# Kernel optimization log

Measured on AMD Instinct MI355X. Metric: run time of the kernel, lower is better.

The kernel has to match this reference:

```python
import jax, jax.numpy as jnp
import numpy as np

T = 128        # number of time points
D = 64         # flattened state dim (bs * z_dim, bs = 1)
H = 256        # hidden width of f-network
HK = 128       # hidden width of kernel network
MAX_IT = 3     # fixed-point iterations (args.max_iterations)


def setup_inputs() -> dict:
    key = jax.random.key(0)
    ks = jax.random.split(key, 6)
    g = lambda k, sh, sc: (jax.random.normal(k, sh, jnp.float32) * sc)
    z0 = jax.random.normal(ks[0], (1, D), jnp.float32)
    t = jnp.linspace(0.0, 1.0, T, dtype=jnp.float32)
    # f: D -> H -> D MLP (the 'func' integrand network)
    W1 = g(ks[1], (D, H), 1.0 / np.sqrt(D)); b1 = jnp.zeros((H,), jnp.float32)
    W2 = g(ks[2], (H, D), 1.0 / np.sqrt(H)); b2 = jnp.zeros((D,), jnp.float32)
    # kernel: (x, s) -> D*D matrix entries (the neural kernel K)
    Wk1 = g(ks[3], (2, HK), 1.0 / np.sqrt(2.0)); bk1 = jnp.zeros((HK,), jnp.float32)
    Wk2 = g(ks[4], (HK, D * D), 1.0 / np.sqrt(HK)); bk2 = jnp.zeros((D * D,), jnp.float32)
    return dict(z0=z0, t=t, W1=W1, b1=b1, W2=W2, b2=b2,
                Wk1=Wk1, bk1=bk1, Wk2=Wk2, bk2=bk2)


def _trapezoid_weights(t):
    """w[i, j]: trapezoid quadrature weight of node j for integral over [t0, t_i]."""
    dt = t[1] - t[0]  # uniform grid
    idx = jnp.arange(T)
    mask = (idx[None, :] <= idx[:, None]).astype(t.dtype)
    w = dt * mask
    w = w.at[(idx, idx)].multiply(0.5)   # halve right endpoint of each row
    w = w.at[:, 0].multiply(0.5)         # halve left endpoint
    w = w.at[0].set(0.0)                 # zero-length integral at t0
    return w


def _solve(z0, t, W1, b1, W2, b2, Wk1, bk1, Wk2, bk2):
    y0 = z0.reshape(-1)                                   # [D], solver flattens batch
    w = _trapezoid_weights(t)                             # [T, T]
    # Neural kernel K(x_i, s_j) -> [D, D], precomputed once on the grid.
    pairs = jnp.stack([jnp.broadcast_to(t[:, None], (T, T)),
                       jnp.broadcast_to(t[None, :], (T, T))], axis=-1)  # [T, T, 2]
    hK = jnp.tanh(pairs @ Wk1 + bk1)                      # [T, T, HK]
    K = (hK @ Wk2 + bk2).reshape(T, T, D, D)              # [T, T, D, D]

    def f(y):  # integrand network, applied over all time points
        return jnp.tanh(y @ W1 + b1) @ W2 + b2            # [T, D]

    def step(y, _):
        # G_i = \int_0^{x_i} K(x_i, s) f(y(s)) ds  (trapezoid on grid)
        G = jnp.einsum('ij,ijde,je->id', w, K, f(y))      # [T, D]
        # y'(x) = G(x)  =>  y_i = y0 + \int_0^{x_i} G(s) ds
        y_new = y0[None, :] + w @ G                       # [T, D]
        return y_new, None

    y_init = jnp.tile(y0[None, :], (T, 1))                # fixed-point initial guess
    y, _ = jax.lax.scan(step, y_init, None, length=MAX_IT)
    return y


def reference(z0, t, W1, b1, W2, b2, Wk1, bk1, Wk2, bk2):
    y = _solve(z0, t, W1, b1, W2, b2, Wk1, bk1, Wk2, bk2)  # [T, D]
    return y[-1].reshape(1, D)  # z[-1]: final state, shape [bs, dim]
```

## Files before the change

### kernel.cpp

```cpp
#include <hip/hip_runtime.h>
#include <hip/hip_bf16.h>

#define TT 128
#define DD 64
#define HH 256
#define HK 128
#define JH (TT*HK)
#define HD (HK*DD)
#define NCHUNK 64

__global__ void __launch_bounds__(256)
k_F0M0(const float* __restrict__ z0,
       const float* __restrict__ W1, const float* __restrict__ b1,
       const float* __restrict__ W2, const float* __restrict__ b2,
       const float* __restrict__ bk2, const float* __restrict__ Wk2,
       float* __restrict__ M0, float* __restrict__ bF0) {
    int bx = blockIdx.x, tid = threadIdx.x;
    int part = tid >> 6, d = tid & 63;
    __shared__ float red[4][64];
    __shared__ float ys[DD];
    __shared__ float hs[HH];
    __shared__ __attribute__((aligned(16))) float fs[DD];
    if (tid < DD) ys[tid] = z0[tid];
    __syncthreads();
    float acc = b1[tid];
    #pragma unroll 8
    for (int e = 0; e < DD; ++e) acc += ys[e] * W1[e * HH + tid];
    hs[tid] = tanhf(acc);
    __syncthreads();
    {
        float s = 0.f;
        #pragma unroll 8
        for (int h = part * 64; h < part * 64 + 64; ++h) s += hs[h] * W2[h * DD + d];
        red[part][d] = s;
    }
    __syncthreads();
    if (part == 0)
        fs[d] = b2[d] + red[0][d] + red[1][d] + red[2][d] + red[3][d];
    __syncthreads();
    if (bx == 0) {
        float s = 0.f;
        #pragma unroll
        for (int e = part * 16; e < part * 16 + 16; ++e) s += bk2[d * DD + e] * fs[e];
        red[part][d] = s;
        __syncthreads();
        if (part == 0)
            bF0[d] = red[0][d] + red[1][d] + red[2][d] + red[3][d];
    }
    int hd = bx * 256 + tid;
    const float* Wrow = Wk2 + (size_t)(hd >> 6) * (DD * DD) + (size_t)(hd & 63) * DD;
    float a = 0.f;
    #pragma unroll
    for (int e = 0; e < DD; e += 8) {
        float4 wa = *(const float4*)(Wrow + e);
        float4 wb = *(const float4*)(Wrow + e + 4);
        float4 fa = *(const float4*)&fs[e];
        float4 fb = *(const float4*)&fs[e + 4];
        a += fa.x*wa.x + fa.y*wa.y + fa.z*wa.z + fa.w*wa.w
           + fb.x*wb.x + fb.y*wb.y + fb.z*wb.z + fb.w*wb.w;
    }
    M0[hd] = a;
}

__global__ void __launch_bounds__(256)
k_G0(const float* __restrict__ t, const float* __restrict__ Wk1,
     const float* __restrict__ bk1, const float* __restrict__ M0,
     const float* __restrict__ bF0, float* __restrict__ G) {
    int i = blockIdx.x, tid = threadIdx.x;
    int part = tid >> 6, d = tid & 63;
    __shared__ float Bpart[2][HK];
    __shared__ float Bs[HK];
    __shared__ float red[4][64];
    float dt = t[1] - t[0];
    int h = tid & 127, half = tid >> 7;
    float b = 0.f;
    if (i > 0) {
        float wk0 = Wk1[h], wk1v = Wk1[HK + h], bk = bk1[h];
        float ti = t[i];
        for (int j = half; j <= i; j += 2) {
            float w = dt * ((j == 0 || j == i) ? 0.5f : 1.0f);
            b += w * tanhf(ti * wk0 + t[j] * wk1v + bk);
        }
    }
    Bpart[half][h] = b;
    __syncthreads();
    if (tid < HK) Bs[tid] = Bpart[0][tid] + Bpart[1][tid];
    __syncthreads();
    float a = 0.f;
    #pragma unroll 8
    for (int h2 = part * 32; h2 < part * 32 + 32; ++h2)
        a += Bs[h2] * M0[h2 * DD + d];
    red[part][d] = a;
    __syncthreads();
    if (part == 0) {
        float g = red[0][d] + red[1][d] + red[2][d] + red[3][d];
        if (i > 0) g += dt * (float)i * bF0[d];
        G[i * DD + d] = g;
    }
}

__global__ void __launch_bounds__(256)
k_F(const float* __restrict__ G, const float* __restrict__ z0,
    const float* __restrict__ t,
    const float* __restrict__ W1, const float* __restrict__ b1,
    const float* __restrict__ W2, const float* __restrict__ b2,
    const float* __restrict__ bk2,
    float* __restrict__ F, float* __restrict__ bF) {
    int j = blockIdx.x, tid = threadIdx.x;
    int part = tid >> 6, d = tid & 63;
    __shared__ float red[4][64];
    __shared__ float ys[DD];
    __shared__ float hs[HH];
    __shared__ float fs[DD];
    float dt = t[1] - t[0];
    {
        float s = 0.f;
        if (j > 0) {
            for (int jp = part; jp <= j; jp += 4) {
                float w = (jp == 0 || jp == j) ? 0.5f : 1.0f;
                s += w * G[jp * DD + d];
            }
        }
        red[part][d] = s;
        __syncthreads();
        if (part == 0)
            ys[d] = z0[d] + dt * (red[0][d] + red[1][d] + red[2][d] + red[3][d]);
    }
    __syncthreads();
    float acc = b1[tid];
    #pragma unroll 8
    for (int e = 0; e < DD; ++e) acc += ys[e] * W1[e * HH + tid];
    hs[tid] = tanhf(acc);
    __syncthreads();
    {
        float s = 0.f;
        #pragma unroll 8
        for (int h = part * 64; h < part * 64 + 64; ++h) s += hs[h] * W2[h * DD + d];
        red[part][d] = s;
    }
    __syncthreads();
    if (part == 0) {
        float a = b2[d] + red[0][d] + red[1][d] + red[2][d] + red[3][d];
        fs[d] = a;
        F[j * DD + d] = a;
    }
    __syncthreads();
    {
        float s = 0.f;
        #pragma unroll
        for (int e = part * 16; e < part * 16 + 16; ++e) s += bk2[d * DD + e] * fs[e];
        red[part][d] = s;
    }
    __syncthreads();
    if (part == 0)
        bF[j * DD + d] = red[0][d] + red[1][d] + red[2][d] + red[3][d];
}

__global__ void __launch_bounds__(256)
k_M(const float* __restrict__ F, const float* __restrict__ Wk2,
    float* __restrict__ M) {
    int tid = threadIdx.x;
    int hd = blockIdx.x * 256 + tid;
    int j0 = blockIdx.y * 8;
    __shared__ __attribute__((aligned(16))) float Fs[8][64];
    for (int k = tid; k < 8 * DD; k += 256) Fs[k >> 6][k & 63] = F[j0 * DD + k];
    __syncthreads();
    float acc[8] = {0.f,0.f,0.f,0.f,0.f,0.f,0.f,0.f};
    const float* Wrow = Wk2 + (size_t)(hd >> 6) * (DD * DD) + (size_t)(hd & 63) * DD;
    for (int e = 0; e < DD; e += 8) {
        float4 wa = *(const float4*)(Wrow + e);
        float4 wb = *(const float4*)(Wrow + e + 4);
        #pragma unroll
        for (int r = 0; r < 8; ++r) {
            float4 f0 = *(const float4*)&Fs[r][e];
            float4 f1 = *(const float4*)&Fs[r][e + 4];
            acc[r] += f0.x*wa.x + f0.y*wa.y + f0.z*wa.z + f0.w*wa.w
                    + f1.x*wb.x + f1.y*wb.y + f1.z*wb.z + f1.w*wb.w;
        }
    }
    #pragma unroll
    for (int r = 0; r < 8; ++r) M[(size_t)(j0 + r) * HD + hd] = acc[r];
}

__global__ void __launch_bounds__(256)
k_G1(const float* __restrict__ t, const float* __restrict__ Wk1,
     const float* __restrict__ bk1, const float* __restrict__ M,
     float* __restrict__ P, const float* __restrict__ z0,
     float* __restrict__ out, int final_it) {
    int itile = blockIdx.x, c = blockIdx.y;
    if (c > 4 * itile + 3) return;
    __shared__ __attribute__((aligned(16))) float As[8 * 256];
    __shared__ float red[4][8][64];
    int tid = threadIdx.x, sub = tid >> 6, d = tid & 63;

    {
        float dt = t[1] - t[0];
        int h = tid & 127;
        int j = 2 * c + (tid >> 7);
        float wk0 = Wk1[h], wk1v = Wk1[HK + h], bk = bk1[h];
        float tj = t[j];
        #pragma unroll
        for (int k = 0; k < 8; ++k) {
            int i = itile * 8 + k;
            float w = (i == 0 || j > i) ? 0.f : dt * ((j == 0 || j == i) ? 0.5f : 1.0f);
            As[k * 256 + tid] = w * tanhf(t[i] * wk0 + tj * wk1v + bk);
        }
    }
    if (final_it && itile == 0 && c == 0 && tid < DD) out[tid] = z0[tid];
    __syncthreads();

    float acc[8] = {0.f,0.f,0.f,0.f,0.f,0.f,0.f,0.f};
    const float* Mp = M + ((size_t)c * 256) * DD + d;
    int jl0 = sub * 64;
    for (int jl = jl0; jl < jl0 + 64; jl += 8) {
        float m0 = Mp[(size_t)(jl + 0) * DD];
        float m1 = Mp[(size_t)(jl + 1) * DD];
        float m2 = Mp[(size_t)(jl + 2) * DD];
        float m3 = Mp[(size_t)(jl + 3) * DD];
        float m4 = Mp[(size_t)(jl + 4) * DD];
        float m5 = Mp[(size_t)(jl + 5) * DD];
        float m6 = Mp[(size_t)(jl + 6) * DD];
        float m7 = Mp[(size_t)(jl + 7) * DD];
        #pragma unroll
        for (int r = 0; r < 8; ++r) {
            float4 a0 = *(const float4*)&As[r * 256 + jl];
            float4 a1 = *(const float4*)&As[r * 256 + jl + 4];
            acc[r] += a0.x*m0 + a0.y*m1 + a0.z*m2 + a0.w*m3
                    + a1.x*m4 + a1.y*m5 + a1.z*m6 + a1.w*m7;
        }
    }
    #pragma unroll
    for (int r = 0; r < 8; ++r) red[sub][r][d] = acc[r];
    __syncthreads();
    if (sub == 0) {
        #pragma unroll
        for (int r = 0; r < 8; ++r) {
            float v = red[0][r][d] + red[1][r][d] + red[2][r][d] + red[3][r][d];
            P[(size_t)c * (TT * DD) + (itile * 8 + r) * DD + d] = v;
        }
    }
}

__global__ void __launch_bounds__(256)
k_Gfin(const float* __restrict__ P, const float* __restrict__ bF,
       const float* __restrict__ t, float* __restrict__ G,
       float* __restrict__ out, int final_it) {
    int j = blockIdx.x, tid = threadIdx.x;
    int part = tid >> 6, d = tid & 63;
    __shared__ float red[4][64];
    float dt = t[1] - t[0];
    float a = 0.f;
    int cmax = j >> 1;
    for (int c = part; c <= cmax; c += 4) a += P[(size_t)c * (TT * DD) + j * DD + d];
    if (j > 0) {
        float s = 0.f;
        for (int jp = part; jp <= j; jp += 4) {
            float w = (jp == 0 || jp == j) ? 0.5f : 1.0f;
            s += w * bF[jp * DD + d];
        }
        a += dt * s;
    }
    red[part][d] = a;
    __syncthreads();
    if (part == 0) {
        float v = red[0][d] + red[1][d] + red[2][d] + red[3][d];
        G[j * DD + d] = v;
        if (final_it) {
            float wj = (j == 0 || j == TT - 1) ? 0.5f : 1.0f;
            atomicAdd(&out[d], dt * wj * v);
        }
    }
}

extern "C" void kernel_launch(void* const* d_in, const int* in_sizes, int n_in,
                              void* d_out, int out_size, void* d_ws, size_t ws_size,
                              hipStream_t stream) {
    const float* z0  = (const float*)d_in[0];
    const float* t   = (const float*)d_in[1];
    const float* W1  = (const float*)d_in[2];
    const float* b1  = (const float*)d_in[3];
    const float* W2  = (const float*)d_in[4];
    const float* b2  = (const float*)d_in[5];
    const float* Wk1 = (const float*)d_in[6];
    const float* bk1 = (const float*)d_in[7];
    const float* Wk2 = (const float*)d_in[8];
    const float* bk2 = (const float*)d_in[9];
    float* out = (float*)d_out;

    float* ws  = (float*)d_ws;
    float* M   = ws;
    float* F   = M   + (size_t)TT*HK*DD;
    float* bF  = F   + TT*DD;
    float* G   = bF  + TT*DD;
    float* P   = G   + TT*DD;
    float* M0  = P   + (size_t)NCHUNK*TT*DD;
    float* bF0 = M0  + HD;

    k_F0M0<<<32, 256, 0, stream>>>(z0, W1, b1, W2, b2, bk2, Wk2, M0, bF0);
    k_G0<<<TT, 256, 0, stream>>>(t, Wk1, bk1, M0, bF0, G);
    for (int it = 1; it < 3; ++it) {
        int fin = (it == 2) ? 1 : 0;
        k_F<<<TT, 256, 0, stream>>>(G, z0, t, W1, b1, W2, b2, bk2, F, bF);
        k_M<<<dim3(32, 16), 256, 0, stream>>>(F, Wk2, M);
        k_G1<<<dim3(16, NCHUNK), 256, 0, stream>>>(t, Wk1, bk1, M, P, z0, out, fin);
        k_Gfin<<<TT, 256, 0, stream>>>(P, bF, t, G, out, fin);
    }
}
```

Measured before the change: 185.7 us.

## Fuse all stages into one cooperative persistent kernel with grid syncs

Replaces the sequence of ten kernel launches with a single cooperative kernel of 256 blocks that moves between stages using grid-wide barriers. The tanh kernel-feature tensor A (T×T×HK) is now computed once up front and kept in workspace, so the G0 and G1 stages read it instead of recomputing tanh in every iteration. The aim is to remove launch overhead and the repeated transcendental work. In exchange it adds grid.sync costs, a large extra workspace buffer that must be read back from memory, and less parallelism in some stages because of the fixed block count. The old multi-kernel path stays as a fallback if the cooperative launch fails.

```diff
diff --git a/kernel.cpp b/kernel.cpp
--- a/kernel.cpp
+++ b/kernel.cpp
@@ -1,13 +1,254 @@
 #include <hip/hip_runtime.h>
-#include <hip/hip_bf16.h>
+#include <hip/hip_cooperative_groups.h>
+
+namespace cg = cooperative_groups;
 
 #define TT 128
 #define DD 64
 #define HH 256
-#define HK 128
-#define JH (TT*HK)
-#define HD (HK*DD)
+#define HKD 128
+#define HD (HKD*DD)
 #define NCHUNK 64
+#define NBLK 256
+
+union __attribute__((aligned(16))) SharedU {
+    struct { float red[4][64]; float ys[DD]; float hs[HH]; float fs[DD]; } f;
+    struct { float Bpart[2][HKD]; float Bs[HKD]; float red[4][64]; } g0;
+    struct { float Fs[8][DD]; } m;
+    struct { float As[8 * 256]; float red[4][8][64]; } g1;
+};
+
+__device__ __forceinline__ void mlp_f(SharedU& sm, int tid,
+                                      const float* __restrict__ W1, const float* __restrict__ b1,
+                                      const float* __restrict__ W2, const float* __restrict__ b2) {
+    int part = tid >> 6, d = tid & 63;
+    float acc = b1[tid];
+    #pragma unroll 8
+    for (int e = 0; e < DD; ++e) acc += sm.f.ys[e] * W1[e * HH + tid];
+    sm.f.hs[tid] = tanhf(acc);
+    __syncthreads();
+    float s = 0.f;
+    #pragma unroll 8
+    for (int h = part * 64; h < part * 64 + 64; ++h) s += sm.f.hs[h] * W2[h * DD + d];
+    sm.f.red[part][d] = s;
+    __syncthreads();
+    if (part == 0)
+        sm.f.fs[d] = b2[d] + sm.f.red[0][d] + sm.f.red[1][d] + sm.f.red[2][d] + sm.f.red[3][d];
+    __syncthreads();
+}
+
+__device__ __forceinline__ float bk2dot(SharedU& sm, int tid, const float* __restrict__ bk2) {
+    int part = tid >> 6, d = tid & 63;
+    float s = 0.f;
+    #pragma unroll
+    for (int e = part * 16; e < part * 16 + 16; ++e) s += bk2[d * DD + e] * sm.f.fs[e];
+    sm.f.red[part][d] = s;
+    __syncthreads();
+    return sm.f.red[0][d] + sm.f.red[1][d] + sm.f.red[2][d] + sm.f.red[3][d];
+}
+
+extern "C" __global__ void __launch_bounds__(256, 2)
+mega(const float* __restrict__ z0, const float* __restrict__ t,
+     const float* __restrict__ W1, const float* __restrict__ b1,
+     const float* __restrict__ W2, const float* __restrict__ b2,
+     const float* __restrict__ Wk1, const float* __restrict__ bk1,
+     const float* __restrict__ Wk2, const float* __restrict__ bk2,
+     float* __restrict__ A, float* __restrict__ M,
+     float* __restrict__ F, float* __restrict__ bF,
+     float* __restrict__ G, float* __restrict__ P,
+     float* __restrict__ M0, float* __restrict__ bF0,
+     float* __restrict__ out)
+{
+    cg::grid_group grid = cg::this_grid();
+    const int b = blockIdx.x, tid = threadIdx.x;
+    const int part = tid >> 6, d = tid & 63;
+    __shared__ SharedU sm;
+    const float dt = t[1] - t[0];
+
+    if (b < 32) {
+        if (tid < DD) sm.f.ys[tid] = z0[tid];
+        __syncthreads();
+        mlp_f(sm, tid, W1, b1, W2, b2);
+        if (b == 0) {
+            float v = bk2dot(sm, tid, bk2);
+            if (part == 0) bF0[d] = v;
+        }
+        int hd = b * 256 + tid;
+        const float* Wrow = Wk2 + (size_t)(hd >> 6) * (DD * DD) + (size_t)(hd & 63) * DD;
+        float a = 0.f;
+        #pragma unroll
+        for (int e = 0; e < DD; e += 8) {
+            float4 wa = *(const float4*)(Wrow + e);
+            float4 wb = *(const float4*)(Wrow + e + 4);
+            float4 fa = *(const float4*)&sm.f.fs[e];
+            float4 fb = *(const float4*)&sm.f.fs[e + 4];
+            a += fa.x*wa.x + fa.y*wa.y + fa.z*wa.z + fa.w*wa.w
+               + fb.x*wb.x + fb.y*wb.y + fb.z*wb.z + fb.w*wb.w;
+        }
+        M0[hd] = a;
+    }
+    {
+        const int h = tid & 127;
+        const float wk0 = Wk1[h], wk1v = Wk1[HKD + h], bk = bk1[h];
+        const int base = b * (TT * TT * HKD / NBLK);
+        #pragma unroll 4
+        for (int k = 0; k < TT * TT * HKD / NBLK / 256; ++k) {
+            int n = base + k * 256 + tid;
+            int i = n >> 14, j = (n >> 7) & 127;
+            float w = (i == 0 || j > i) ? 0.f : dt * ((j == 0 || j == i) ? 0.5f : 1.f);
+            float v = 0.f;
+            if (w != 0.f)
+                v = w * tanhf(t[i] * wk0 + t[j] * wk1v + bk);
+            A[n] = v;
+        }
+    }
+    grid.sync();
+
+    if (b < TT) {
+        const int i = b;
+        const int h = tid & 127, half = tid >> 7;
+        float bsum = 0.f;
+        const float* Ai = A + (size_t)i * (TT * HKD);
+        for (int j = half; j <= i; j += 2) bsum += Ai[j * HKD + h];
+        sm.g0.Bpart[half][h] = bsum;
+        __syncthreads();
+        if (tid < HKD) sm.g0.Bs[tid] = sm.g0.Bpart[0][tid] + sm.g0.Bpart[1][tid];
+        __syncthreads();
+        float a = 0.f;
+        #pragma unroll 8
+        for (int h2 = part * 32; h2 < part * 32 + 32; ++h2) a += sm.g0.Bs[h2] * M0[h2 * DD + d];
+        sm.g0.red[part][d] = a;
+        __syncthreads();
+        if (part == 0) {
+            float g = sm.g0.red[0][d] + sm.g0.red[1][d] + sm.g0.red[2][d] + sm.g0.red[3][d];
+            if (i > 0) g += dt * (float)i * bF0[d];
+            G[i * DD + d] = g;
+        }
+    }
+    grid.sync();
+
+    for (int it = 1; it < 3; ++it) {
+        const int fin = (it == 2);
+
+        if (b < TT) {
+            const int j = b;
+            float s = 0.f;
+            if (j > 0) {
+                for (int jp = part; jp <= j; jp += 4) {
+                    float w = (jp == 0 || jp == j) ? 0.5f : 1.0f;
+                    s += w * G[jp * DD + d];
+                }
+            }
+            sm.f.red[part][d] = s;
+            __syncthreads();
+            if (part == 0)
+                sm.f.ys[d] = z0[d] + dt * (sm.f.red[0][d] + sm.f.red[1][d] + sm.f.red[2][d] + sm.f.red[3][d]);
+            __syncthreads();
+            mlp_f(sm, tid, W1, b1, W2, b2);
+            if (part == 0) F[j * DD + d] = sm.f.fs[d];
+            float v = bk2dot(sm, tid, bk2);
+            if (part == 0) bF[j * DD + d] = v;
+        }
+        grid.sync();
+
+        for (int u = b; u < 512; u += NBLK) {
+            const int hd = (u & 31) * 256 + tid;
+            const int j0 = (u >> 5) * 8;
+            __syncthreads();
+            for (int k2 = tid; k2 < 8 * DD; k2 += 256) sm.m.Fs[k2 >> 6][k2 & 63] = F[j0 * DD + k2];
+            __syncthreads();
+            float acc[8] = {0.f,0.f,0.f,0.f,0.f,0.f,0.f,0.f};
+            const float* Wrow = Wk2 + (size_t)(hd >> 6) * (DD * DD) + (size_t)(hd & 63) * DD;
+            for (int e = 0; e < DD; e += 8) {
+                float4 wa = *(const float4*)(Wrow + e);
+                float4 wb = *(const float4*)(Wrow + e + 4);
+                #pragma unroll
+                for (int r = 0; r < 8; ++r) {
+                    float4 f0 = *(const float4*)&sm.m.Fs[r][e];
+                    float4 f1 = *(const float4*)&sm.m.Fs[r][e + 4];
+                    acc[r] += f0.x*wa.x + f0.y*wa.y + f0.z*wa.z + f0.w*wa.w
+                            + f1.x*wb.x + f1.y*wb.y + f1.z*wb.z + f1.w*wb.w;
+                }
+            }
+            #pragma unroll
+            for (int r = 0; r < 8; ++r) M[(size_t)(j0 + r) * HD + hd] = acc[r];
+        }
+        grid.sync();
+
+        if (fin && b == 0 && tid < DD) out[tid] = z0[tid];
+        for (int u = b; u < 544; u += NBLK) {
+            int uu = u, itile = 0;
+            while (uu >= 4 * (itile + 1)) { uu -= 4 * (itile + 1); ++itile; }
+            const int c = uu;
+            __syncthreads();
+            const float* Asrc = A + ((size_t)(itile * 8) * TT + 2 * c) * HKD;
+            for (int q = tid; q < 8 * 64; q += 256) {
+                int r = q >> 6, c4 = q & 63;
+                ((float4*)sm.g1.As)[r * 64 + c4] =
+                    *(const float4*)(Asrc + (size_t)r * TT * HKD + c4 * 4);
+            }
+            __syncthreads();
+            float acc[8] = {0.f,0.f,0.f,0.f,0.f,0.f,0.f,0.f};
+            const float* Mp = M + ((size_t)c * 256) * DD + d;
+            const int jl0 = part * 64;
+            for (int jl = jl0; jl < jl0 + 64; jl += 8) {
+                float m0 = Mp[(size_t)(jl + 0) * DD];
+                float m1 = Mp[(size_t)(jl + 1) * DD];
+                float m2 = Mp[(size_t)(jl + 2) * DD];
+                float m3 = Mp[(size_t)(jl + 3) * DD];
+                float m4 = Mp[(size_t)(jl + 4) * DD];
+                float m5 = Mp[(size_t)(jl + 5) * DD];
+                float m6 = Mp[(size_t)(jl + 6) * DD];
+                float m7 = Mp[(size_t)(jl + 7) * DD];
+                #pragma unroll
+                for (int r = 0; r < 8; ++r) {
+                    float4 a0 = *(const float4*)&sm.g1.As[r * 256 + jl];
+                    float4 a1 = *(const float4*)&sm.g1.As[r * 256 + jl + 4];
+                    acc[r] += a0.x*m0 + a0.y*m1 + a0.z*m2 + a0.w*m3
+                            + a1.x*m4 + a1.y*m5 + a1.z*m6 + a1.w*m7;
+                }
+            }
+            #pragma unroll
+            for (int r = 0; r < 8; ++r) sm.g1.red[part][r][d] = acc[r];
+            __syncthreads();
+            if (part == 0) {
+                #pragma unroll
+                for (int r = 0; r < 8; ++r) {
+                    float v = sm.g1.red[0][r][d] + sm.g1.red[1][r][d]
+                            + sm.g1.red[2][r][d] + sm.g1.red[3][r][d];
+                    P[(size_t)c * (TT * DD) + (itile * 8 + r) * DD + d] = v;
+                }
+            }
+        }
+        grid.sync();
+
+        if (b < TT) {
+            const int j = b;
+            float a = 0.f;
+            const int cmax = j >> 1;
+            for (int c = part; c <= cmax; c += 4) a += P[(size_t)c * (TT * DD) + j * DD + d];
+            if (j > 0) {
+                float s2 = 0.f;
+                for (int jp = part; jp <= j; jp += 4) {
+                    float w = (jp == 0 || jp == j) ? 0.5f : 1.0f;
+                    s2 += w * bF[jp * DD + d];
+                }
+                a += dt * s2;
+            }
+            sm.f.red[part][d] = a;
+            __syncthreads();
+            if (part == 0) {
+                float v = sm.f.red[0][d] + sm.f.red[1][d] + sm.f.red[2][d] + sm.f.red[3][d];
+                G[j * DD + d] = v;
+                if (fin) {
+                    float wj = (j == 0 || j == TT - 1) ? 0.5f : 1.0f;
+                    atomicAdd(&out[d], dt * wj * v);
+                }
+            }
+        }
+        if (it == 1) grid.sync();
+    }
+}
 
 __global__ void __launch_bounds__(256)
 k_F0M0(const float* __restrict__ z0,
@@ -68,14 +309,14 @@
      const float* __restrict__ bF0, float* __restrict__ G) {
     int i = blockIdx.x, tid = threadIdx.x;
     int part = tid >> 6, d = tid & 63;
-    __shared__ float Bpart[2][HK];
-    __shared__ float Bs[HK];
+    __shared__ float Bpart[2][HKD];
+    __shared__ float Bs[HKD];
     __shared__ float red[4][64];
     float dt = t[1] - t[0];
     int h = tid & 127, half = tid >> 7;
     float b = 0.f;
     if (i > 0) {
-        float wk0 = Wk1[h], wk1v = Wk1[HK + h], bk = bk1[h];
+        float wk0 = Wk1[h], wk1v = Wk1[HKD + h], bk = bk1[h];
         float ti = t[i];
         for (int j = half; j <= i; j += 2) {
             float w = dt * ((j == 0 || j == i) ? 0.5f : 1.0f);
@@ -84,7 +325,7 @@
     }
     Bpart[half][h] = b;
     __syncthreads();
-    if (tid < HK) Bs[tid] = Bpart[0][tid] + Bpart[1][tid];
+    if (tid < HKD) Bs[tid] = Bpart[0][tid] + Bpart[1][tid];
     __syncthreads();
     float a = 0.f;
     #pragma unroll 8
@@ -192,12 +433,11 @@
     __shared__ __attribute__((aligned(16))) float As[8 * 256];
     __shared__ float red[4][8][64];
     int tid = threadIdx.x, sub = tid >> 6, d = tid & 63;
-
     {
         float dt = t[1] - t[0];
         int h = tid & 127;
         int j = 2 * c + (tid >> 7);
-        float wk0 = Wk1[h], wk1v = Wk1[HK + h], bk = bk1[h];
+        float wk0 = Wk1[h], wk1v = Wk1[HKD + h], bk = bk1[h];
         float tj = t[j];
         #pragma unroll
         for (int k = 0; k < 8; ++k) {
@@ -208,7 +448,6 @@
     }
     if (final_it && itile == 0 && c == 0 && tid < DD) out[tid] = z0[tid];
     __syncthreads();
-
     float acc[8] = {0.f,0.f,0.f,0.f,0.f,0.f,0.f,0.f};
     const float* Mp = M + ((size_t)c * 256) * DD + d;
     int jl0 = sub * 64;
@@ -288,13 +527,30 @@
     float* out = (float*)d_out;
 
     float* ws  = (float*)d_ws;
-    float* M   = ws;
-    float* F   = M   + (size_t)TT*HK*DD;
+    float* A   = ws;
+    float* M   = A   + (size_t)TT*TT*HKD;
+    float* F   = M   + (size_t)TT*HKD*DD;
     float* bF  = F   + TT*DD;
     float* G   = bF  + TT*DD;
     float* P   = G   + TT*DD;
     float* M0  = P   + (size_t)NCHUNK*TT*DD;
     float* bF0 = M0  + HD;
+
+    static int use_coop = -1;
+
+    if (use_coop != 0) {
+        void* args[] = {
+            (void*)&z0, (void*)&t, (void*)&W1, (void*)&b1, (void*)&W2, (void*)&b2,
+            (void*)&Wk1, (void*)&bk1, (void*)&Wk2, (void*)&bk2,
+            (void*)&A, (void*)&M, (void*)&F, (void*)&bF, (void*)&G, (void*)&P,
+            (void*)&M0, (void*)&bF0, (void*)&out
+        };
+        hipError_t e = hipLaunchCooperativeKernel((const void*)mega, dim3(NBLK),
+                                                  dim3(256), args, 0, stream);
+        if (e == hipSuccess) { use_coop = 1; return; }
+        (void)hipGetLastError();
+        use_coop = 0;
+    }
 
     k_F0M0<<<32, 256, 0, stream>>>(z0, W1, b1, W2, b2, bk2, Wk2, M0, bF0);
     k_G0<<<TT, 256, 0, stream>>>(t, Wk1, bk1, M0, bF0, G);
```

Result: slower. 459.4 us (+147.4%).

## Fuse all stages into one persistent kernel with software grid barriers

Applied to the files above, without the earlier changes.

Replaces the ten separate kernel launches with a single persistent kernel of 512 blocks that moves between stages through a flag-based global barrier. It also computes the weighted tanh kernel-feature tensor A once into global memory, so later stages load it instead of recomputing tanh each iteration. The G1 stage now walks only the valid triangular tiles in a flattened loop. The aim is to cut launch overhead and repeated transcendental work, at the cost of spin-wait barrier latency, a memset, a large extra workspace buffer, and the assumption that all 512 blocks are co-resident.

```diff
diff --git a/kernel.cpp b/kernel.cpp
--- a/kernel.cpp
+++ b/kernel.cpp
@@ -1,274 +1,273 @@
 #include <hip/hip_runtime.h>
-#include <hip/hip_bf16.h>
 
 #define TT 128
 #define DD 64
 #define HH 256
-#define HK 128
-#define JH (TT*HK)
-#define HD (HK*DD)
-#define NCHUNK 64
-
-__global__ void __launch_bounds__(256)
-k_F0M0(const float* __restrict__ z0,
-       const float* __restrict__ W1, const float* __restrict__ b1,
-       const float* __restrict__ W2, const float* __restrict__ b2,
-       const float* __restrict__ bk2, const float* __restrict__ Wk2,
-       float* __restrict__ M0, float* __restrict__ bF0) {
-    int bx = blockIdx.x, tid = threadIdx.x;
+#define HKD 128
+#define HD (HKD*DD)
+#define NB 512
+
+union __attribute__((aligned(16))) SharedU {
+    struct { float red[4][64]; float ys[DD]; float hs[HH]; float fs[DD]; } f;
+    struct { float Bpart[2][HKD]; float Bs[HKD]; float red[4][64]; } g0;
+    struct { float Fs[8][DD]; } m;
+    struct { float As[8 * 256]; float red[4][8][64]; } g1;
+};
+
+__device__ __forceinline__ void gbar(int* flags, int* go, int gen, int b, int tid) {
+    __syncthreads();
+    if (tid == 0) {
+        __builtin_amdgcn_fence(__ATOMIC_RELEASE, "agent");
+        __hip_atomic_store(&flags[b], gen, __ATOMIC_RELAXED, __HIP_MEMORY_SCOPE_AGENT);
+    }
+    if (b == 0) {
+        bool ok;
+        do {
+            int v1 = __hip_atomic_load(&flags[tid],       __ATOMIC_RELAXED, __HIP_MEMORY_SCOPE_AGENT);
+            int v2 = __hip_atomic_load(&flags[tid + 256], __ATOMIC_RELAXED, __HIP_MEMORY_SCOPE_AGENT);
+            ok = (v1 >= gen) && (v2 >= gen);
+            if (!ok) __builtin_amdgcn_s_sleep(1);
+        } while (!__syncthreads_and(ok));
+        if (tid == 0)
+            __hip_atomic_store(go, gen, __ATOMIC_RELAXED, __HIP_MEMORY_SCOPE_AGENT);
+    } else if (tid == 0) {
+        while (__hip_atomic_load(go, __ATOMIC_RELAXED, __HIP_MEMORY_SCOPE_AGENT) < gen)
+            __builtin_amdgcn_s_sleep(2);
+    }
+    __syncthreads();
+    __builtin_amdgcn_fence(__ATOMIC_ACQUIRE, "agent");
+}
+
+__device__ __forceinline__ void mlp_f(SharedU& sm, int tid,
+                                      const float* __restrict__ W1, const float* __restrict__ b1,
+                                      const float* __restrict__ W2, const float* __restrict__ b2) {
     int part = tid >> 6, d = tid & 63;
-    __shared__ float red[4][64];
-    __shared__ float ys[DD];
-    __shared__ float hs[HH];
-    __shared__ __attribute__((aligned(16))) float fs[DD];
-    if (tid < DD) ys[tid] = z0[tid];
-    __syncthreads();
     float acc = b1[tid];
     #pragma unroll 8
-    for (int e = 0; e < DD; ++e) acc += ys[e] * W1[e * HH + tid];
-    hs[tid] = tanhf(acc);
-    __syncthreads();
+    for (int e = 0; e < DD; ++e) acc += sm.f.ys[e] * W1[e * HH + tid];
+    sm.f.hs[tid] = tanhf(acc);
+    __syncthreads();
+    float s = 0.f;
+    #pragma unroll 8
+    for (int h = part * 64; h < part * 64 + 64; ++h) s += sm.f.hs[h] * W2[h * DD + d];
+    sm.f.red[part][d] = s;
+    __syncthreads();
+    if (part == 0)
+        sm.f.fs[d] = b2[d] + sm.f.red[0][d] + sm.f.red[1][d] + sm.f.red[2][d] + sm.f.red[3][d];
+    __syncthreads();
+}
+
+__device__ __forceinline__ float bk2dot(SharedU& sm, int tid, const float* __restrict__ bk2) {
+    int part = tid >> 6, d = tid & 63;
+    float s = 0.f;
+    #pragma unroll
+    for (int e = part * 16; e < part * 16 + 16; ++e) s += bk2[d * DD + e] * sm.f.fs[e];
+    sm.f.red[part][d] = s;
+    __syncthreads();
+    return sm.f.red[0][d] + sm.f.red[1][d] + sm.f.red[2][d] + sm.f.red[3][d];
+}
+
+extern "C" __global__ void __launch_bounds__(256, 2)
+mega(const float* __restrict__ z0, const float* __restrict__ t,
+     const float* __restrict__ W1, const float* __restrict__ b1,
+     const float* __restrict__ W2, const float* __restrict__ b2,
+     const float* __restrict__ Wk1, const float* __restrict__ bk1,
+     const float* __restrict__ Wk2, const float* __restrict__ bk2,
+     float* __restrict__ A, float* __restrict__ M,
+     float* __restrict__ F, float* __restrict__ bF,
+     float* __restrict__ G, float* __restrict__ P,
+     float* __restrict__ M0, float* __restrict__ bF0,
+     int* flags, int* go, float* __restrict__ out)
+{
+    const int b = blockIdx.x, tid = threadIdx.x;
+    const int part = tid >> 6, d = tid & 63;
+    __shared__ SharedU sm;
+    const float dt = t[1] - t[0];
+    int gen = 0;
+
+    if (b < 32) {
+        if (tid < DD) sm.f.ys[tid] = z0[tid];
+        __syncthreads();
+        mlp_f(sm, tid, W1, b1, W2, b2);
+        if (b == 0) {
+            float v = bk2dot(sm, tid, bk2);
+            if (part == 0) bF0[d] = v;
+        }
+        int hd = b * 256 + tid;
+        const float* Wrow = Wk2 + (size_t)(hd >> 6) * (DD * DD) + (size_t)(hd & 63) * DD;
+        float a = 0.f;
+        #pragma unroll
+        for (int e = 0; e < DD; e += 8) {
+            float4 wa = *(const float4*)(Wrow + e);
+            float4 wb = *(const float4*)(Wrow + e + 4);
+            float4 fa = *(const float4*)&sm.f.fs[e];
+            float4 fb = *(const float4*)&sm.f.fs[e + 4];
+            a += fa.x*wa.x + fa.y*wa.y + fa.z*wa.z + fa.w*wa.w
+               + fb.x*wb.x + fb.y*wb.y + fb.z*wb.z + fb.w*wb.w;
+        }
+        M0[hd] = a;
+    }
     {
-        float s = 0.f;
+        const int h = tid & 127;
+        const float wk0 = Wk1[h], wk1v = Wk1[HKD + h], bk = bk1[h];
+        const int i = b >> 2;
+        const float ti = t[i];
+        const int base = b * 4096;
+        #pragma unroll 4
+        for (int k = 0; k < 16; ++k) {
+            int n = base + k * 256 + tid;
+            int j = (n >> 7) & 127;
+            float w = (i == 0 || j > i) ? 0.f : dt * ((j == 0 || j == i) ? 0.5f : 1.f);
+            float v = 0.f;
+            if (w != 0.f)
+                v = w * tanhf(ti * wk0 + t[j] * wk1v + bk);
+            A[n] = v;
+        }
+    }
+    gbar(flags, go, ++gen, b, tid);
+
+    if (b < TT) {
+        const int i = b;
+        const int h = tid & 127, half = tid >> 7;
+        float bsum = 0.f;
+        const float* Ai = A + (size_t)i * (TT * HKD);
+        for (int j = half; j <= i; j += 2) bsum += Ai[j * HKD + h];
+        sm.g0.Bpart[half][h] = bsum;
+        __syncthreads();
+        if (tid < HKD) sm.g0.Bs[tid] = sm.g0.Bpart[0][tid] + sm.g0.Bpart[1][tid];
+        __syncthreads();
+        float a = 0.f;
         #pragma unroll 8
-        for (int h = part * 64; h < part * 64 + 64; ++h) s += hs[h] * W2[h * DD + d];
-        red[part][d] = s;
-    }
-    __syncthreads();
-    if (part == 0)
-        fs[d] = b2[d] + red[0][d] + red[1][d] + red[2][d] + red[3][d];
-    __syncthreads();
-    if (bx == 0) {
-        float s = 0.f;
-        #pragma unroll
-        for (int e = part * 16; e < part * 16 + 16; ++e) s += bk2[d * DD + e] * fs[e];
-        red[part][d] = s;
+        for (int h2 = part * 32; h2 < part * 32 + 32; ++h2) a += sm.g0.Bs[h2] * M0[h2 * DD + d];
+        sm.g0.red[part][d] = a;
         __syncthreads();
-        if (part == 0)
-            bF0[d] = red[0][d] + red[1][d] + red[2][d] + red[3][d];
-    }
-    int hd = bx * 256 + tid;
-    const float* Wrow = Wk2 + (size_t)(hd >> 6) * (DD * DD) + (size_t)(hd & 63) * DD;
-    float a = 0.f;
-    #pragma unroll
-    for (int e = 0; e < DD; e += 8) {
-        float4 wa = *(const float4*)(Wrow + e);
-        float4 wb = *(const float4*)(Wrow + e + 4);
-        float4 fa = *(const float4*)&fs[e];
-        float4 fb = *(const float4*)&fs[e + 4];
-        a += fa.x*wa.x + fa.y*wa.y + fa.z*wa.z + fa.w*wa.w
-           + fb.x*wb.x + fb.y*wb.y + fb.z*wb.z + fb.w*wb.w;
-    }
-    M0[hd] = a;
-}
-
-__global__ void __launch_bounds__(256)
-k_G0(const float* __restrict__ t, const float* __restrict__ Wk1,
-     const float* __restrict__ bk1, const float* __restrict__ M0,
-     const float* __restrict__ bF0, float* __restrict__ G) {
-    int i = blockIdx.x, tid = threadIdx.x;
-    int part = tid >> 6, d = tid & 63;
-    __shared__ float Bpart[2][HK];
-    __shared__ float Bs[HK];
-    __shared__ float red[4][64];
-    float dt = t[1] - t[0];
-    int h = tid & 127, half = tid >> 7;
-    float b = 0.f;
-    if (i > 0) {
-        float wk0 = Wk1[h], wk1v = Wk1[HK + h], bk = bk1[h];
-        float ti = t[i];
-        for (int j = half; j <= i; j += 2) {
-            float w = dt * ((j == 0 || j == i) ? 0.5f : 1.0f);
-            b += w * tanhf(ti * wk0 + t[j] * wk1v + bk);
-        }
-    }
-    Bpart[half][h] = b;
-    __syncthreads();
-    if (tid < HK) Bs[tid] = Bpart[0][tid] + Bpart[1][tid];
-    __syncthreads();
-    float a = 0.f;
-    #pragma unroll 8
-    for (int h2 = part * 32; h2 < part * 32 + 32; ++h2)
-        a += Bs[h2] * M0[h2 * DD + d];
-    red[part][d] = a;
-    __syncthreads();
-    if (part == 0) {
-        float g = red[0][d] + red[1][d] + red[2][d] + red[3][d];
-        if (i > 0) g += dt * (float)i * bF0[d];
-        G[i * DD + d] = g;
-    }
-}
-
-__global__ void __launch_bounds__(256)
-k_F(const float* __restrict__ G, const float* __restrict__ z0,
-    const float* __restrict__ t,
-    const float* __restrict__ W1, const float* __restrict__ b1,
-    const float* __restrict__ W2, const float* __restrict__ b2,
-    const float* __restrict__ bk2,
-    float* __restrict__ F, float* __restrict__ bF) {
-    int j = blockIdx.x, tid = threadIdx.x;
-    int part = tid >> 6, d = tid & 63;
-    __shared__ float red[4][64];
-    __shared__ float ys[DD];
-    __shared__ float hs[HH];
-    __shared__ float fs[DD];
-    float dt = t[1] - t[0];
-    {
-        float s = 0.f;
-        if (j > 0) {
-            for (int jp = part; jp <= j; jp += 4) {
-                float w = (jp == 0 || jp == j) ? 0.5f : 1.0f;
-                s += w * G[jp * DD + d];
-            }
-        }
-        red[part][d] = s;
-        __syncthreads();
-        if (part == 0)
-            ys[d] = z0[d] + dt * (red[0][d] + red[1][d] + red[2][d] + red[3][d]);
-    }
-    __syncthreads();
-    float acc = b1[tid];
-    #pragma unroll 8
-    for (int e = 0; e < DD; ++e) acc += ys[e] * W1[e * HH + tid];
-    hs[tid] = tanhf(acc);
-    __syncthreads();
-    {
-        float s = 0.f;
-        #pragma unroll 8
-        for (int h = part * 64; h < part * 64 + 64; ++h) s += hs[h] * W2[h * DD + d];
-        red[part][d] = s;
-    }
-    __syncthreads();
-    if (part == 0) {
-        float a = b2[d] + red[0][d] + red[1][d] + red[2][d] + red[3][d];
-        fs[d] = a;
-        F[j * DD + d] = a;
-    }
-    __syncthreads();
-    {
-        float s = 0.f;
-        #pragma unroll
-        for (int e = part * 16; e < part * 16 + 16; ++e) s += bk2[d * DD + e] * fs[e];
-        red[part][d] = s;
-    }
-    __syncthreads();
-    if (part == 0)
-        bF[j * DD + d] = red[0][d] + red[1][d] + red[2][d] + red[3][d];
-}
-
-__global__ void __launch_bounds__(256)
-k_M(const float* __restrict__ F, const float* __restrict__ Wk2,
-    float* __restrict__ M) {
-    int tid = threadIdx.x;
-    int hd = blockIdx.x * 256 + tid;
-    int j0 = blockIdx.y * 8;
-    __shared__ __attribute__((aligned(16))) float Fs[8][64];
-    for (int k = tid; k < 8 * DD; k += 256) Fs[k >> 6][k & 63] = F[j0 * DD + k];
-    __syncthreads();
-    float acc[8] = {0.f,0.f,0.f,0.f,0.f,0.f,0.f,0.f};
-    const float* Wrow = Wk2 + (size_t)(hd >> 6) * (DD * DD) + (size_t)(hd & 63) * DD;
-    for (int e = 0; e < DD; e += 8) {
-        float4 wa = *(const float4*)(Wrow + e);
-        float4 wb = *(const float4*)(Wrow + e + 4);
-        #pragma unroll
-        for (int r = 0; r < 8; ++r) {
-            float4 f0 = *(const float4*)&Fs[r][e];
-            float4 f1 = *(const float4*)&Fs[r][e + 4];
-            acc[r] += f0.x*wa.x + f0.y*wa.y + f0.z*wa.z + f0.w*wa.w
-                    + f1.x*wb.x + f1.y*wb.y + f1.z*wb.z + f1.w*wb.w;
-        }
-    }
-    #pragma unroll
-    for (int r = 0; r < 8; ++r) M[(size_t)(j0 + r) * HD + hd] = acc[r];
-}
-
-__global__ void __launch_bounds__(256)
-k_G1(const float* __restrict__ t, const float* __restrict__ Wk1,
-     const float* __restrict__ bk1, const float* __restrict__ M,
-     float* __restrict__ P, const float* __restrict__ z0,
-     float* __restrict__ out, int final_it) {
-    int itile = blockIdx.x, c = blockIdx.y;
-    if (c > 4 * itile + 3) return;
-    __shared__ __attribute__((aligned(16))) float As[8 * 256];
-    __shared__ float red[4][8][64];
-    int tid = threadIdx.x, sub = tid >> 6, d = tid & 63;
-
-    {
-        float dt = t[1] - t[0];
-        int h = tid & 127;
-        int j = 2 * c + (tid >> 7);
-        float wk0 = Wk1[h], wk1v = Wk1[HK + h], bk = bk1[h];
-        float tj = t[j];
-        #pragma unroll
-        for (int k = 0; k < 8; ++k) {
-            int i = itile * 8 + k;
-            float w = (i == 0 || j > i) ? 0.f : dt * ((j == 0 || j == i) ? 0.5f : 1.0f);
-            As[k * 256 + tid] = w * tanhf(t[i] * wk0 + tj * wk1v + bk);
-        }
-    }
-    if (final_it && itile == 0 && c == 0 && tid < DD) out[tid] = z0[tid];
-    __syncthreads();
-
-    float acc[8] = {0.f,0.f,0.f,0.f,0.f,0.f,0.f,0.f};
-    const float* Mp = M + ((size_t)c * 256) * DD + d;
-    int jl0 = sub * 64;
-    for (int jl = jl0; jl < jl0 + 64; jl += 8) {
-        float m0 = Mp[(size_t)(jl + 0) * DD];
-        float m1 = Mp[(size_t)(jl + 1) * DD];
-        float m2 = Mp[(size_t)(jl + 2) * DD];
-        float m3 = Mp[(size_t)(jl + 3) * DD];
-        float m4 = Mp[(size_t)(jl + 4) * DD];
-        float m5 = Mp[(size_t)(jl + 5) * DD];
-        float m6 = Mp[(size_t)(jl + 6) * DD];
-        float m7 = Mp[(size_t)(jl + 7) * DD];
-        #pragma unroll
-        for (int r = 0; r < 8; ++r) {
-            float4 a0 = *(const float4*)&As[r * 256 + jl];
-            float4 a1 = *(const float4*)&As[r * 256 + jl + 4];
-            acc[r] += a0.x*m0 + a0.y*m1 + a0.z*m2 + a0.w*m3
-                    + a1.x*m4 + a1.y*m5 + a1.z*m6 + a1.w*m7;
-        }
-    }
-    #pragma unroll
-    for (int r = 0; r < 8; ++r) red[sub][r][d] = acc[r];
-    __syncthreads();
-    if (sub == 0) {
-        #pragma unroll
-        for (int r = 0; r < 8; ++r) {
-            float v = red[0][r][d] + red[1][r][d] + red[2][r][d] + red[3][r][d];
-            P[(size_t)c * (TT * DD) + (itile * 8 + r) * DD + d] = v;
-        }
-    }
-}
-
-__global__ void __launch_bounds__(256)
-k_Gfin(const float* __restrict__ P, const float* __restrict__ bF,
-       const float* __restrict__ t, float* __restrict__ G,
-       float* __restrict__ out, int final_it) {
-    int j = blockIdx.x, tid = threadIdx.x;
-    int part = tid >> 6, d = tid & 63;
-    __shared__ float red[4][64];
-    float dt = t[1] - t[0];
-    float a = 0.f;
-    int cmax = j >> 1;
-    for (int c = part; c <= cmax; c += 4) a += P[(size_t)c * (TT * DD) + j * DD + d];
-    if (j > 0) {
-        float s = 0.f;
-        for (int jp = part; jp <= j; jp += 4) {
-            float w = (jp == 0 || jp == j) ? 0.5f : 1.0f;
-            s += w * bF[jp * DD + d];
-        }
-        a += dt * s;
-    }
-    red[part][d] = a;
-    __syncthreads();
-    if (part == 0) {
-        float v = red[0][d] + red[1][d] + red[2][d] + red[3][d];
-        G[j * DD + d] = v;
-        if (final_it) {
-            float wj = (j == 0 || j == TT - 1) ? 0.5f : 1.0f;
-            atomicAdd(&out[d], dt * wj * v);
-        }
+        if (part == 0) {
+            float g = sm.g0.red[0][d] + sm.g0.red[1][d] + sm.g0.red[2][d] + sm.g0.red[3][d];
+            if (i > 0) g += dt * (float)i * bF0[d];
+            G[i * DD + d] = g;
+        }
+    }
+    gbar(flags, go, ++gen, b, tid);
+
+    for (int it = 1; it < 3; ++it) {
+        const int fin = (it == 2);
+
+        if (b < TT) {
+            const int j = b;
+            float s = 0.f;
+            if (j > 0) {
+                for (int jp = part; jp <= j; jp += 4) {
+                    float w = (jp == 0 || jp == j) ? 0.5f : 1.0f;
+                    s += w * G[jp * DD + d];
+                }
+            }
+            sm.f.red[part][d] = s;
+            __syncthreads();
+            if (part == 0)
+                sm.f.ys[d] = z0[d] + dt * (sm.f.red[0][d] + sm.f.red[1][d] + sm.f.red[2][d] + sm.f.red[3][d]);
+            __syncthreads();
+            mlp_f(sm, tid, W1, b1, W2, b2);
+            if (part == 0) F[j * DD + d] = sm.f.fs[d];
+            float v = bk2dot(sm, tid, bk2);
+            if (part == 0) bF[j * DD + d] = v;
+        }
+        gbar(flags, go, ++gen, b, tid);
+
+        {
+            const int hd = (b & 31) * 256 + tid;
+            const int j0 = (b >> 5) * 8;
+            for (int k2 = tid; k2 < 8 * DD; k2 += 256) sm.m.Fs[k2 >> 6][k2 & 63] = F[j0 * DD + k2];
+            __syncthreads();
+            float acc[8] = {0.f,0.f,0.f,0.f,0.f,0.f,0.f,0.f};
+            const float* Wrow = Wk2 + (size_t)(hd >> 6) * (DD * DD) + (size_t)(hd & 63) * DD;
+            for (int e = 0; e < DD; e += 8) {
+                float4 wa = *(const float4*)(Wrow + e);
+                float4 wb = *(const float4*)(Wrow + e + 4);
+                #pragma unroll
+                for (int r = 0; r < 8; ++r) {
+                    float4 f0 = *(const float4*)&sm.m.Fs[r][e];
+                    float4 f1 = *(const float4*)&sm.m.Fs[r][e + 4];
+                    acc[r] += f0.x*wa.x + f0.y*wa.y + f0.z*wa.z + f0.w*wa.w
+                            + f1.x*wb.x + f1.y*wb.y + f1.z*wb.z + f1.w*wb.w;
+                }
+            }
+            #pragma unroll
+            for (int r = 0; r < 8; ++r) M[(size_t)(j0 + r) * HD + hd] = acc[r];
+        }
+        gbar(flags, go, ++gen, b, tid);
+
+        if (fin && b == 0 && tid < DD) out[tid] = z0[tid];
+        for (int u = b; u < 544; u += NB) {
+            int uu = u, itile = 0;
+            while (uu >= 4 * (itile + 1)) { uu -= 4 * (itile + 1); ++itile; }
+            const int c = uu;
+            __syncthreads();
+            const float* Asrc = A + ((size_t)(itile * 8) * TT + 2 * c) * HKD;
+            for (int q = tid; q < 8 * 64; q += 256) {
+                int r = q >> 6, c4 = q & 63;
+                ((float4*)sm.g1.As)[r * 64 + c4] =
+                    *(const float4*)(Asrc + (size_t)r * TT * HKD + c4 * 4);
+            }
+            __syncthreads();
+            float acc[8] = {0.f,0.f,0.f,0.f,0.f,0.f,0.f,0.f};
+            const float* Mp = M + ((size_t)c * 256) * DD + d;
+            const int jl0 = part * 64;
+            for (int jl = jl0; jl < jl0 + 64; jl += 8) {
+                float m0 = Mp[(size_t)(jl + 0) * DD];
+                float m1 = Mp[(size_t)(jl + 1) * DD];
+                float m2 = Mp[(size_t)(jl + 2) * DD];
+                float m3 = Mp[(size_t)(jl + 3) * DD];
+                float m4 = Mp[(size_t)(jl + 4) * DD];
+                float m5 = Mp[(size_t)(jl + 5) * DD];
+                float m6 = Mp[(size_t)(jl + 6) * DD];
+                float m7 = Mp[(size_t)(jl + 7) * DD];
+                #pragma unroll
+                for (int r = 0; r < 8; ++r) {
+                    float4 a0 = *(const float4*)&sm.g1.As[r * 256 + jl];
+                    float4 a1 = *(const float4*)&sm.g1.As[r * 256 + jl + 4];
+                    acc[r] += a0.x*m0 + a0.y*m1 + a0.z*m2 + a0.w*m3
+                            + a1.x*m4 + a1.y*m5 + a1.z*m6 + a1.w*m7;
+                }
+            }
+            #pragma unroll
+            for (int r = 0; r < 8; ++r) sm.g1.red[part][r][d] = acc[r];
+            __syncthreads();
+            if (part == 0) {
+                #pragma unroll
+                for (int r = 0; r < 8; ++r) {
+                    float v = sm.g1.red[0][r][d] + sm.g1.red[1][r][d]
+                            + sm.g1.red[2][r][d] + sm.g1.red[3][r][d];
+                    P[(size_t)c * (TT * DD) + (itile * 8 + r) * DD + d] = v;
+                }
+            }
+        }
+        gbar(flags, go, ++gen, b, tid);
+
+        if (b < TT) {
+            const int j = b;
+            float a = 0.f;
+            const int cmax = j >> 1;
+            for (int c = part; c <= cmax; c += 4) a += P[(size_t)c * (TT * DD) + j * DD + d];
+            if (j > 0) {
+                float s2 = 0.f;
+                for (int jp = part; jp <= j; jp += 4) {
+                    float w = (jp == 0 || jp == j) ? 0.5f : 1.0f;
+                    s2 += w * bF[jp * DD + d];
+                }
+                a += dt * s2;
+            }
+            sm.f.red[part][d] = a;
+            __syncthreads();
+            if (part == 0) {
+                float v = sm.f.red[0][d] + sm.f.red[1][d] + sm.f.red[2][d] + sm.f.red[3][d];
+                G[j * DD + d] = v;
+                if (fin) {
+                    float wj = (j == 0 || j == TT - 1) ? 0.5f : 1.0f;
+                    atomicAdd(&out[d], dt * wj * v);
+                }
+            }
+        }
+        if (it == 1) gbar(flags, go, ++gen, b, tid);
     }
 }
 
@@ -288,21 +287,24 @@
     float* out = (float*)d_out;
 
     float* ws  = (float*)d_ws;
-    float* M   = ws;
-    float* F   = M   + (size_t)TT*HK*DD;
+    float* A   = ws;
+    float* M   = A   + (size_t)TT*TT*HKD;
+    float* F   = M   + (size_t)TT*HKD*DD;
     float* bF  = F   + TT*DD;
     float* G   = bF  + TT*DD;
     float* P   = G   + TT*DD;
-    float* M0  = P   + (size_t)NCHUNK*TT*DD;
+    float* M0  = P   + (size_t)64*TT*DD;
     float* bF0 = M0  + HD;
-
-    k_F0M0<<<32, 256, 0, stream>>>(z0, W1, b1, W2, b2, bk2, Wk2, M0, bF0);
-    k_G0<<<TT, 256, 0, stream>>>(t, Wk1, bk1, M0, bF0, G);
-    for (int it = 1; it < 3; ++it) {
-        int fin = (it == 2) ? 1 : 0;
-        k_F<<<TT, 256, 0, stream>>>(G, z0, t, W1, b1, W2, b2, bk2, F, bF);
-        k_M<<<dim3(32, 16), 256, 0, stream>>>(F, Wk2, M);
-        k_G1<<<dim3(16, NCHUNK), 256, 0, stream>>>(t, Wk1, bk1, M, P, z0, out, fin);
-        k_Gfin<<<TT, 256, 0, stream>>>(P, bF, t, G, out, fin);
-    }
-}
+    int*   flags = (int*)(bF0 + DD);
+    int*   go    = flags + NB;
+
+    hipMemsetAsync(flags, 0, (NB + 1) * sizeof(int), stream);
+
+    void* args[] = {
+        (void*)&z0, (void*)&t, (void*)&W1, (void*)&b1, (void*)&W2, (void*)&b2,
+        (void*)&Wk1, (void*)&bk1, (void*)&Wk2, (void*)&bk2,
+        (void*)&A, (void*)&M, (void*)&F, (void*)&bF, (void*)&G, (void*)&P,
+        (void*)&M0, (void*)&bF0, (void*)&flags, (void*)&go, (void*)&out
+    };
+    hipLaunchKernel((const void*)mega, dim3(NB), dim3(256), args, 0, stream);
+}
```

New measurement: 391.5 us. 2.11x slower.
